# Optimization experiments

Measured on AMD Instinct MI355X. Metric: run time of the kernel, lower is better.

The kernel has to match this reference:

```python
import jax, jax.numpy as jnp
import numpy as np

B, T, C = 8, 2048, 2048   # batch, seq, embedding
A = 2048                  # attn_dim
H, N = 32, 64             # heads, head_size
LORA_MIX, LORA_DEC = 32, 64
EPS = 1e-5 * 8 ** 2       # GroupNorm eps with head_size_divisor=8


def setup_inputs() -> dict:
    key = jax.random.key(0)
    ks = jax.random.split(key, 24)
    s = lambda k, shape, scale=1.0: jax.random.normal(k, shape, jnp.float32) * scale
    inp = {
        'x': s(ks[0], (B, T, C)),
        'time_maa_x': jax.random.uniform(ks[1], (1, 1, C)),
        'time_maa_w': jax.random.uniform(ks[2], (1, 1, C)),
        'time_maa_k': jax.random.uniform(ks[3], (1, 1, C)),
        'time_maa_v': jax.random.uniform(ks[4], (1, 1, C)),
        'time_maa_r': jax.random.uniform(ks[5], (1, 1, C)),
        'time_maa_g': jax.random.uniform(ks[6], (1, 1, C)),
        'maa_w1': s(ks[7], (C, LORA_MIX * 5), 0.01),
        'maa_w2': s(ks[8], (5, LORA_MIX, C), 0.01),
        'time_decay': s(ks[9], (1, 1, A)) - 4.0,   # decay_speed init is in [-6,-1]
        'decay_w1': s(ks[10], (C, LORA_DEC), 0.01),
        'decay_w2': s(ks[11], (LORA_DEC, A), 0.01),
        'u': s(ks[12], (H, N), 0.1),
        'Wr': s(ks[13], (A, C), C ** -0.5),
        'Wk': s(ks[14], (A, C), C ** -0.5),
        'Wv': s(ks[15], (A, C), C ** -0.5),
        'Wg': s(ks[16], (A, C), C ** -0.5),
        'Wo': s(ks[17], (C, A), A ** -0.5),
        'ln_w': jnp.ones((A,), jnp.float32),
        'ln_b': jnp.zeros((A,), jnp.float32),
    }
    return inp


def wkv6(r, k, v, dec, u):
    # r,k,v,dec: (B,T,A) -> (T,B,H,N); dec already exp(-exp(w))
    def to_tbhn(a):
        return a.reshape(B, T, H, N).transpose(1, 0, 2, 3)
    rr, kk, vv, dd = map(to_tbhn, (r, k, v, dec))

    def step(S, inp):  # S: (B,H,N,N) indexed [key_chan i, val_chan j]
        rt, kt, vt, dt = inp
        a = kt[..., :, None] * vt[..., None, :]            # rank-1 update (B,H,N,N)
        y = jnp.einsum('bhi,bhij->bhj', rt, S + u[None, :, :, None] * a)
        S = dt[..., None] * S + a                          # per-key-channel decay
        return S, y

    S0 = jnp.zeros((B, H, N, N), r.dtype)
    _, y = jax.lax.scan(step, S0, (rr, kk, vv, dd))
    return y.transpose(1, 0, 2, 3).reshape(B, T, A)


def reference(x, time_maa_x, time_maa_w, time_maa_k, time_maa_v, time_maa_r,
              time_maa_g, maa_w1, maa_w2, time_decay, decay_w1, decay_w2,
              u, Wr, Wk, Wv, Wg, Wo, ln_w, ln_b):
    # token shift: x[t-1] - x[t] (zero-padded at t=0)
    xx = jnp.pad(x, ((0, 0), (1, 0), (0, 0)))[:, :T] - x
    xxx = x + xx * time_maa_x
    m = jnp.tanh(xxx @ maa_w1).reshape(B, T, 5, LORA_MIX)
    m = jnp.einsum('btfd,fdc->fbtc', m, maa_w2)            # (5,B,T,C)
    mw, mk, mv, mr, mg = m

    xw = x + xx * (time_maa_w + mw)
    xk = x + xx * (time_maa_k + mk)
    xv = x + xx * (time_maa_v + mv)
    xr = x + xx * (time_maa_r + mr)
    xg = x + xx * (time_maa_g + mg)

    r = xr @ Wr.T
    k = xk @ Wk.T
    v = xv @ Wv.T
    g = jax.nn.silu(xg @ Wg.T)
    w = time_decay + jnp.tanh(xw @ decay_w1) @ decay_w2
    dec = jnp.exp(-jnp.exp(w))                              # RWKV6 decay mapping

    y = wkv6(r, k, v, dec, u)

    # GroupNorm over each head's N channels
    yg = y.reshape(B, T, H, N)
    mu = yg.mean(-1, keepdims=True)
    var = yg.var(-1, keepdims=True)
    yn = ((yg - mu) * jax.lax.rsqrt(var + EPS)).reshape(B, T, A)
    yn = yn * ln_w + ln_b

    return (yn * g) @ Wo.T
```

## Files before the change

kernel.cpp:

```cpp
#include <hip/hip_runtime.h>
#include <hip/hip_bf16.h>
#include <cstdint>
#include <cstddef>

#define B_ 8
#define T_ 2048
#define C_ 2048
#define A_ 2048
#define H_ 32
#define BT_ (B_*T_)

typedef short short8 __attribute__((ext_vector_type(8)));
typedef _Float16 half8 __attribute__((ext_vector_type(8)));
typedef float floatx4 __attribute__((ext_vector_type(4)));

__device__ __forceinline__ unsigned short f2bf(float f) {
  union { float f; uint32_t u; } a; a.f = f;
  uint32_t r = a.u + 0x7fffu + ((a.u >> 16) & 1u);
  return (unsigned short)(r >> 16);
}
__device__ __forceinline__ float bf2f(unsigned short s) {
  union { uint32_t u; float f; } a; a.u = ((uint32_t)s) << 16;
  return a.f;
}
__device__ __forceinline__ unsigned short f2h(float f) {
  union { _Float16 h; unsigned short u; } c; c.h = (_Float16)f; return c.u;
}
__device__ __forceinline__ float h2f(unsigned short u) {
  union { unsigned short u; _Float16 h; } c; c.u = u; return (float)c.h;
}
__device__ __forceinline__ void split_hl(float v, unsigned short& hh, unsigned short& ll) {
  hh = f2bf(v);
  ll = f2bf(v - bf2f(hh));
}
__device__ __forceinline__ int swz(int row, int col) {
  return row * 64 + (col ^ ((row & 7) << 3));
}
__device__ __forceinline__ short8 ldfrag(const unsigned short* M, int row, int col8) {
  return *(const short8*)&M[row * 64 + (col8 ^ ((row & 7) << 3))];
}

__global__ void conv_f16(const float* __restrict__ s, unsigned short* __restrict__ d, int n) {
  int i = blockIdx.x * 256 + threadIdx.x;
  if (i < n) d[i] = f2h(s[i]);
}

__global__ void transpose_pad(const float* __restrict__ s, unsigned short* __restrict__ d, int NP, int NV) {
  int i = blockIdx.x * 256 + threadIdx.x;
  int n = i >> 11, kk = i & 2047;
  if (n < NP) d[i] = (n < NV) ? f2h(s[kk * NV + n]) : (unsigned short)0;
}

__global__ void transpose_w2(const float* __restrict__ s, unsigned short* __restrict__ d) {
  int i = blockIdx.x * 256 + threadIdx.x;
  int f = i >> 16, rem = i & 65535;
  int dd = rem >> 11, c = rem & 2047;
  d[((size_t)(f * 2048 + c) << 5) + dd] = f2h(s[((size_t)(f * 32 + dd) << 11) + c]);
}

__global__ void shift_mix(const float* __restrict__ x, const float* __restrict__ tmx,
                          unsigned short* __restrict__ xxx) {
  size_t i4 = (size_t)blockIdx.x * 256 + threadIdx.x;
  size_t i = i4 * 4;
  int c = (int)(i & 2047);
  int t = (int)((i >> 11) & 2047);
  float4 xv = *(const float4*)&x[i];
  float4 pv = make_float4(0.f, 0.f, 0.f, 0.f);
  if (t > 0) pv = *(const float4*)&x[i - 2048];
  float4 tv = *(const float4*)&tmx[c];
  ushort4 m;
  m.x = f2h(xv.x + (pv.x - xv.x) * tv.x);
  m.y = f2h(xv.y + (pv.y - xv.y) * tv.y);
  m.z = f2h(xv.z + (pv.z - xv.z) * tv.z);
  m.w = f2h(xv.w + (pv.w - xv.w) * tv.w);
  *(ushort4*)&xxx[i] = m;
}

__device__ __forceinline__ void gll16(const void* g, void* l) {
  __builtin_amdgcn_global_load_lds(
      (const __attribute__((address_space(1))) void*)g,
      (__attribute__((address_space(3))) void*)l, 16, 0, 0);
}

template<int EPI>
__global__ __launch_bounds__(256)
void gemm_f16(const unsigned short* __restrict__ Am, const unsigned short* __restrict__ Bm,
              void* __restrict__ Cp, int M, int N, int K) {
  __shared__ unsigned short As[128 * 32];
  __shared__ unsigned short Bs[128 * 32];
  const int tid = threadIdx.x;
  const int wid = tid >> 6, lane = tid & 63;
  const int quad = lane >> 4, l15 = lane & 15;
  const long bm = (long)blockIdx.x * 128, bn = (long)blockIdx.y * 128;
  const int wm = (wid & 1) * 64, wn = (wid >> 1) * 64;

  floatx4 acc[4][4];
#pragma unroll
  for (int a = 0; a < 4; a++)
#pragma unroll
    for (int b = 0; b < 4; b++) { floatx4 z = {0.f, 0.f, 0.f, 0.f}; acc[a][b] = z; }

  const int stg_row = wid * 32 + (lane >> 2);
  const int stg_k   = (lane & 3) * 8;
  const int stg_lds = wid * 1024 + lane * 8;

  for (int k0 = 0; k0 < K; k0 += 32) {
    __syncthreads();
#pragma unroll
    for (int p = 0; p < 2; ++p) {
      gll16(Am + (bm + stg_row + p * 16) * (long)K + k0 + stg_k, &As[stg_lds + p * 512]);
      gll16(Bm + (bn + stg_row + p * 16) * (long)K + k0 + stg_k, &Bs[stg_lds + p * 512]);
    }
    __syncthreads();

    half8 af[4], bfr[4];
#pragma unroll
    for (int mi = 0; mi < 4; mi++) af[mi] = *(const half8*)&As[(wm + mi * 16 + l15) * 32 + quad * 8];
#pragma unroll
    for (int ni = 0; ni < 4; ni++) bfr[ni] = *(const half8*)&Bs[(wn + ni * 16 + l15) * 32 + quad * 8];
#pragma unroll
    for (int mi = 0; mi < 4; mi++)
#pragma unroll
      for (int ni = 0; ni < 4; ni++)
        acc[mi][ni] = __builtin_amdgcn_mfma_f32_16x16x32_f16(af[mi], bfr[ni], acc[mi][ni], 0, 0, 0);
  }

#pragma unroll
  for (int mi = 0; mi < 4; mi++)
#pragma unroll
    for (int ni = 0; ni < 4; ni++)
#pragma unroll
      for (int vv = 0; vv < 4; ++vv) {
        long row = bm + wm + mi * 16 + quad * 4 + vv;
        long col = bn + wn + ni * 16 + l15;
        float val = acc[mi][ni][vv];
        if (EPI == 0) {
          ((unsigned short*)Cp)[row * N + col] = f2bf(val);
        } else if (EPI == 1) {
          float s = val / (1.f + __expf(-val));
          ((unsigned short*)Cp)[row * N + col] = f2h(s);
        } else if (EPI == 2) {
          ((float*)Cp)[row * N + col] = tanhf(val);
        } else if (EPI == 4) {
          ((unsigned short*)Cp)[row * N + col] = f2h(tanhf(val));
        } else {
          ((float*)Cp)[row * N + col] = val;
        }
      }
}

__global__ __launch_bounds__(256)
void mix_gemm(const unsigned short* __restrict__ m5f, const unsigned short* __restrict__ w2T,
              const float* __restrict__ x,
              const float* __restrict__ tmw, const float* __restrict__ tmk,
              const float* __restrict__ tmv, const float* __restrict__ tmr,
              const float* __restrict__ tmg,
              unsigned short* __restrict__ xw, unsigned short* __restrict__ xk,
              unsigned short* __restrict__ xv, unsigned short* __restrict__ xr,
              unsigned short* __restrict__ xg) {
  __shared__ unsigned short As[128 * 32];
  __shared__ unsigned short Bs[128 * 32];
  const int tid = threadIdx.x;
  const int wid = tid >> 6, lane = tid & 63;
  const int quad = lane >> 4, l15 = lane & 15;
  const long bm = (long)blockIdx.x * 128, bn = (long)blockIdx.y * 128;
  const int f = blockIdx.z;
  const int wm = (wid & 1) * 64, wn = (wid >> 1) * 64;

  const float* tmf = (f == 0) ? tmw : (f == 1) ? tmk : (f == 2) ? tmv : (f == 3) ? tmr : tmg;
  unsigned short* outf = (f == 0) ? xw : (f == 1) ? xk : (f == 2) ? xv : (f == 3) ? xr : xg;

  const int stg_row = wid * 32 + (lane >> 2);
  const int stg_k   = (lane & 3) * 8;
  const int stg_lds = wid * 1024 + lane * 8;

#pragma unroll
  for (int p = 0; p < 2; ++p) {
    gll16(m5f + (bm + stg_row + p * 16) * 256 + f * 32 + stg_k, &As[stg_lds + p * 512]);
    gll16(w2T + ((long)f * 2048 + bn + stg_row + p * 16) * 32 + stg_k, &Bs[stg_lds + p * 512]);
  }
  __syncthreads();

  half8 af[4], bfr[4];
#pragma unroll
  for (int mi = 0; mi < 4; mi++) af[mi] = *(const half8*)&As[(wm + mi * 16 + l15) * 32 + quad * 8];
#pragma unroll
  for (int ni = 0; ni < 4; ni++) bfr[ni] = *(const half8*)&Bs[(wn + ni * 16 + l15) * 32 + quad * 8];

  floatx4 acc[4][4];
#pragma unroll
  for (int a = 0; a < 4; a++)
#pragma unroll
    for (int b = 0; b < 4; b++) { floatx4 z = {0.f, 0.f, 0.f, 0.f}; acc[a][b] = z; }
#pragma unroll
  for (int mi = 0; mi < 4; mi++)
#pragma unroll
    for (int ni = 0; ni < 4; ni++)
      acc[mi][ni] = __builtin_amdgcn_mfma_f32_16x16x32_f16(af[mi], bfr[ni], acc[mi][ni], 0, 0, 0);

#pragma unroll
  for (int ni = 0; ni < 4; ni++) {
    const long col = bn + wn + ni * 16 + l15;
    const float tv = tmf[col];
#pragma unroll
    for (int mi = 0; mi < 4; mi++) {
      const long row0 = bm + wm + mi * 16 + quad * 4;
      const size_t idx0 = (size_t)row0 * 2048 + col;
      float xc[4];
#pragma unroll
      for (int vv = 0; vv < 4; ++vv) xc[vv] = x[idx0 + (size_t)vv * 2048];
      float xprev = ((row0 & 2047) > 0) ? x[idx0 - 2048] : 0.f;
#pragma unroll
      for (int vv = 0; vv < 4; ++vv) {
        const float xp = vv ? xc[vv - 1] : xprev;
        outf[idx0 + (size_t)vv * 2048] = f2h(xc[vv] + (xp - xc[vv]) * (tv + acc[mi][ni][vv]));
      }
    }
  }
}

__global__ __launch_bounds__(256)
void decay_kernel(const float* __restrict__ t1, const float* __restrict__ w2d,
                  const float* __restrict__ td, float* __restrict__ dec) {
  const int bt0 = blockIdx.x * 16;
  const int tid = threadIdx.x;
  for (int cc = 0; cc < 8; ++cc) {
    const int a = cc * 256 + tid;
    const float tda = td[a];
    float acc[16];
#pragma unroll
    for (int b = 0; b < 16; b++) acc[b] = 0.f;
    for (int dc = 0; dc < 16; ++dc) {
      float wv0 = w2d[((size_t)(dc * 4 + 0) << 11) + a];
      float wv1 = w2d[((size_t)(dc * 4 + 1) << 11) + a];
      float wv2 = w2d[((size_t)(dc * 4 + 2) << 11) + a];
      float wv3 = w2d[((size_t)(dc * 4 + 3) << 11) + a];
#pragma unroll
      for (int b = 0; b < 16; b++) {
        float4 mv = *(const float4*)&t1[((size_t)(bt0 + b) << 7) + dc * 4];
        acc[b] += mv.x * wv0 + mv.y * wv1 + mv.z * wv2 + mv.w * wv3;
      }
    }
#pragma unroll
    for (int b = 0; b < 16; b++) {
      dec[((size_t)(bt0 + b) << 11) + a] = __expf(-__expf(tda + acc[b]));
    }
  }
}

template<int KF32>
__global__ __launch_bounds__(512, 1)
void wkv6_chunk(const unsigned short* __restrict__ r, const unsigned short* __restrict__ k16,
                const float* __restrict__ k32, const float* __restrict__ v,
                const float* __restrict__ dec, const float* __restrict__ u,
                unsigned short* __restrict__ gz,
                const float* __restrict__ lnw, const float* __restrict__ lnb) {
  __shared__ unsigned short Rh[4096], Rl[4096];
  __shared__ unsigned short Kh[4096], Kl[4096];
  __shared__ unsigned short KTh[4096], KTl[4096];
  __shared__ unsigned short VTh[4096], VTl[4096];
  __shared__ unsigned short Amh[4096], Aml[4096];
  __shared__ unsigned short SThi[4096], STlo[4096];
  __shared__ float STf[4096];
  __shared__ float qpart[8][64];
  __shared__ float LcEnd[64];
  __shared__ float diagv[64];
  __shared__ float gnp[8][16][2];

  const int bh = blockIdx.x, b = bh >> 5, h = bh & 31;
  const int tid = threadIdx.x;
  const int w = tid >> 6, lane = tid & 63;
  const int quad = lane >> 4, l15 = lane & 15;
  const int cb = h * 64;
  const int wr = w >> 1, wc = w & 1;
  const int rq = w * 8;
  const int mrow = wr * 16;
  const int mcol = wc * 32;

  const float uu = u[cb + lane];
  float lnwv[2], lnbv[2];
#pragma unroll
  for (int ni = 0; ni < 2; ++ni) {
    lnwv[ni] = lnw[cb + mcol + ni * 16 + l15];
    lnbv[ni] = lnb[cb + mcol + ni * 16 + l15];
  }

  for (int i = tid; i < 4096; i += 512) STf[i] = 0.f;

  const size_t bT = (size_t)b * T_;

  float dA[8], rA[8], kA[8], vA[8];
  {
    const size_t ro = (bT + rq) * (size_t)A_ + cb + lane;
#pragma unroll
    for (int q = 0; q < 8; ++q) {
      const size_t o = ro + (size_t)q * A_;
      dA[q] = dec[o];
      rA[q] = bf2f(r[o]);
      if (KF32) kA[q] = k32[o];
      else      kA[q] = bf2f(k16[o]);
      vA[q] = v[o];
    }
  }

  for (int c = 0; c < T_ / 64; ++c) {
    const int t0 = c * 64;
    float lcq[8];
    lcq[0] = dA[0];
#pragma unroll
    for (int q = 1; q < 8; ++q) lcq[q] = lcq[q - 1] * dA[q];
    qpart[w][lane] = lcq[7];
    __syncthreads();
    {
      float pre = 1.f;
#pragma unroll
      for (int pw = 0; pw < 7; ++pw)
        if (pw < w) pre *= qpart[pw][lane];
      if (w == 7) LcEnd[lane] = pre * lcq[7];
      unsigned short hh, ll;
#pragma unroll
      for (int q = 0; q < 8; ++q) {
        const int jr = rq + q;
        split_hl(STf[jr * 64 + lane], hh, ll);
        const int ixs = swz(jr, lane);
        SThi[ixs] = hh; STlo[ixs] = ll;
      }
      short8 ktph, ktpl, vtph, vtpl;
#pragma unroll
      for (int q = 0; q < 8; ++q) {
        const int tr = rq + q;
        const float Pl = q ? pre * lcq[q - 1] : pre;
        const float Lc = pre * lcq[q];
        const int ix = swz(tr, lane);
        split_hl(rA[q] * Pl, hh, ll);
        Rh[ix] = hh; Rl[ix] = ll;
        const float kn = kA[q] / Lc;
        split_hl(kn, hh, ll);
        Kh[ix] = hh; Kl[ix] = ll;
        ktph[q] = (short)hh; ktpl[q] = (short)ll;
        split_hl(vA[q], hh, ll);
        vtph[q] = (short)hh; vtpl[q] = (short)ll;
        float dp = rA[q] * uu * kA[q];
        dp += __shfl_xor(dp, 1, 64);
        dp += __shfl_xor(dp, 2, 64);
        dp += __shfl_xor(dp, 4, 64);
        dp += __shfl_xor(dp, 8, 64);
        dp += __shfl_xor(dp, 16, 64);
        dp += __shfl_xor(dp, 32, 64);
        if (lane == 0) diagv[tr] = dp;
      }
      const int ixT = lane * 64 + (rq ^ ((lane & 7) << 3));
      *(short8*)&KTh[ixT] = ktph;
      *(short8*)&KTl[ixT] = ktpl;
      *(short8*)&VTh[ixT] = vtph;
      *(short8*)&VTl[ixT] = vtpl;
    }
    __syncthreads();
    if (c + 1 < T_ / 64) {
      const size_t ro = (bT + t0 + 64 + rq) * (size_t)A_ + cb + lane;
#pragma unroll
      for (int q = 0; q < 8; ++q) {
        const size_t o = ro + (size_t)q * A_;
        dA[q] = dec[o];
        rA[q] = bf2f(r[o]);
        if (KF32) kA[q] = k32[o];
        else      kA[q] = bf2f(k16[o]);
        vA[q] = v[o];
      }
    }
    {
      short8 arh[2], arl[2];
#pragma unroll
      for (int kst = 0; kst < 2; ++kst) {
        const int c8 = kst * 32 + quad * 8;
        arh[kst] = ldfrag(Rh, mrow + l15, c8);
        arl[kst] = ldfrag(Rl, mrow + l15, c8);
      }
      floatx4 acc[2];
#pragma unroll
      for (int ni = 0; ni < 2; ++ni) { floatx4 z = {0.f, 0.f, 0.f, 0.f}; acc[ni] = z; }
#pragma unroll
      for (int ni = 0; ni < 2; ++ni)
#pragma unroll
        for (int kst = 0; kst < 2; ++kst) {
          const int c8 = kst * 32 + quad * 8;
          short8 bh_ = ldfrag(Kh, mcol + ni * 16 + l15, c8);
          short8 bl_ = ldfrag(Kl, mcol + ni * 16 + l15, c8);
          acc[ni] = __builtin_amdgcn_mfma_f32_16x16x32_bf16(arh[kst], bh_, acc[ni], 0, 0, 0);
          acc[ni] = __builtin_amdgcn_mfma_f32_16x16x32_bf16(arh[kst], bl_, acc[ni], 0, 0, 0);
          acc[ni] = __builtin_amdgcn_mfma_f32_16x16x32_bf16(arl[kst], bh_, acc[ni], 0, 0, 0);
        }
#pragma unroll
      for (int ni = 0; ni < 2; ++ni)
#pragma unroll
        for (int vv = 0; vv < 4; ++vv) {
          const int grow = mrow + quad * 4 + vv;
          const int gcol = mcol + ni * 16 + l15;
          float val = (grow > gcol) ? acc[ni][vv] : ((grow == gcol) ? diagv[grow] : 0.f);
          unsigned short hh, ll;
          split_hl(val, hh, ll);
          const int ix = swz(grow, gcol);
          Amh[ix] = hh; Aml[ix] = ll;
        }
    }
    __syncthreads();
    {
      short8 aAh[2], aAl[2], aRh[2], aRl[2];
#pragma unroll
      for (int kst = 0; kst < 2; ++kst) {
        const int c8 = kst * 32 + quad * 8;
        aAh[kst] = ldfrag(Amh, mrow + l15, c8);
        aAl[kst] = ldfrag(Aml, mrow + l15, c8);
        aRh[kst] = ldfrag(Rh, mrow + l15, c8);
        aRl[kst] = ldfrag(Rl, mrow + l15, c8);
      }
      floatx4 acc[2];
#pragma unroll
      for (int ni = 0; ni < 2; ++ni) { floatx4 z = {0.f, 0.f, 0.f, 0.f}; acc[ni] = z; }
#pragma unroll
      for (int ni = 0; ni < 2; ++ni)
#pragma unroll
        for (int kst = 0; kst < 2; ++kst) {
          const int c8 = kst * 32 + quad * 8;
          const int brow = mcol + ni * 16 + l15;
          short8 bvh = ldfrag(VTh, brow, c8);
          short8 bvl = ldfrag(VTl, brow, c8);
          acc[ni] = __builtin_amdgcn_mfma_f32_16x16x32_bf16(aAh[kst], bvh, acc[ni], 0, 0, 0);
          acc[ni] = __builtin_amdgcn_mfma_f32_16x16x32_bf16(aAh[kst], bvl, acc[ni], 0, 0, 0);
          acc[ni] = __builtin_amdgcn_mfma_f32_16x16x32_bf16(aAl[kst], bvh, acc[ni], 0, 0, 0);
          short8 bsh = ldfrag(SThi, brow, c8);
          short8 bsl = ldfrag(STlo, brow, c8);
          acc[ni] = __builtin_amdgcn_mfma_f32_16x16x32_bf16(aRh[kst], bsh, acc[ni], 0, 0, 0);
          acc[ni] = __builtin_amdgcn_mfma_f32_16x16x32_bf16(aRh[kst], bsl, acc[ni], 0, 0, 0);
          acc[ni] = __builtin_amdgcn_mfma_f32_16x16x32_bf16(aRl[kst], bsh, acc[ni], 0, 0, 0);
        }
      float s1_[4], s2_[4];
#pragma unroll
      for (int vv = 0; vv < 4; ++vv) {
        float s1 = acc[0][vv] + acc[1][vv];
        float s2 = acc[0][vv] * acc[0][vv] + acc[1][vv] * acc[1][vv];
        s1 += __shfl_xor(s1, 1, 64); s2 += __shfl_xor(s2, 1, 64);
        s1 += __shfl_xor(s1, 2, 64); s2 += __shfl_xor(s2, 2, 64);
        s1 += __shfl_xor(s1, 4, 64); s2 += __shfl_xor(s2, 4, 64);
        s1 += __shfl_xor(s1, 8, 64); s2 += __shfl_xor(s2, 8, 64);
        s1_[vv] = s1; s2_[vv] = s2;
        if (l15 == 0) {
          gnp[w][quad * 4 + vv][0] = s1;
          gnp[w][quad * 4 + vv][1] = s2;
        }
      }
      __syncthreads();
#pragma unroll
      for (int ni = 0; ni < 2; ++ni)
#pragma unroll
        for (int vv = 0; vv < 4; ++vv) {
          const int rloc = quad * 4 + vv;
          float s1 = s1_[vv] + gnp[w ^ 1][rloc][0];
          float s2 = s2_[vv] + gnp[w ^ 1][rloc][1];
          float mu = s1 * (1.f / 64.f);
          float var = s2 * (1.f / 64.f) - mu * mu;
          float rs = rsqrtf(var + 6.4e-4f);
          const size_t off = (bT + t0 + mrow + rloc) * (size_t)A_ + cb + mcol + ni * 16 + l15;
          float yn = (acc[ni][vv] - mu) * rs * lnwv[ni] + lnbv[ni];
          float z = yn * h2f(gz[off]);
          gz[off] = f2h(z);
        }
    }
    {
      short8 avh[2], avl[2];
#pragma unroll
      for (int kst = 0; kst < 2; ++kst) {
        const int c8 = kst * 32 + quad * 8;
        avh[kst] = ldfrag(VTh, mrow + l15, c8);
        avl[kst] = ldfrag(VTl, mrow + l15, c8);
      }
      floatx4 a4[2];
#pragma unroll
      for (int ni = 0; ni < 2; ++ni) { floatx4 z = {0.f, 0.f, 0.f, 0.f}; a4[ni] = z; }
#pragma unroll
      for (int ni = 0; ni < 2; ++ni)
#pragma unroll
        for (int kst = 0; kst < 2; ++kst) {
          const int c8 = kst * 32 + quad * 8;
          short8 bkh = ldfrag(KTh, mcol + ni * 16 + l15, c8);
          short8 bkl = ldfrag(KTl, mcol + ni * 16 + l15, c8);
          a4[ni] = __builtin_amdgcn_mfma_f32_16x16x32_bf16(avh[kst], bkh, a4[ni], 0, 0, 0);
          a4[ni] = __builtin_amdgcn_mfma_f32_16x16x32_bf16(avh[kst], bkl, a4[ni], 0, 0, 0);
          a4[ni] = __builtin_amdgcn_mfma_f32_16x16x32_bf16(avl[kst], bkh, a4[ni], 0, 0, 0);
        }
#pragma unroll
      for (int ni = 0; ni < 2; ++ni) {
        const float lce = LcEnd[mcol + ni * 16 + l15];
#pragma unroll
        for (int vv = 0; vv < 4; ++vv) {
          const int jr = mrow + quad * 4 + vv;
          const int ic = mcol + ni * 16 + l15;
          STf[jr * 64 + ic] = lce * (a4[ni][vv] + STf[jr * 64 + ic]);
        }
      }
    }
    __syncthreads();
  }
}

extern "C" void kernel_launch(void* const* d_in, const int* in_sizes, int n_in,
                              void* d_out, int out_size, void* d_ws, size_t ws_size,
                              hipStream_t stream) {
  (void)in_sizes; (void)n_in; (void)out_size;
  const float* x   = (const float*)d_in[0];
  const float* tmx = (const float*)d_in[1];
  const float* tmw = (const float*)d_in[2];
  const float* tmk = (const float*)d_in[3];
  const float* tmv = (const float*)d_in[4];
  const float* tmr = (const float*)d_in[5];
  const float* tmg = (const float*)d_in[6];
  const float* w1  = (const float*)d_in[7];
  const float* w2  = (const float*)d_in[8];
  const float* td  = (const float*)d_in[9];
  const float* dw1 = (const float*)d_in[10];
  const float* dw2 = (const float*)d_in[11];
  const float* u   = (const float*)d_in[12];
  const float* Wr  = (const float*)d_in[13];
  const float* Wk  = (const float*)d_in[14];
  const float* Wv  = (const float*)d_in[15];
  const float* Wg  = (const float*)d_in[16];
  const float* Wo  = (const float*)d_in[17];
  const float* lnw = (const float*)d_in[18];
  const float* lnb = (const float*)d_in[19];

  char* ws = (char*)d_ws;
  const size_t MB = 1024 * 1024;
  unsigned short* xxx  = (unsigned short*)(ws + 0 * MB);
  unsigned short* gb   = (unsigned short*)(ws + 0 * MB);
  unsigned short* m5   = (unsigned short*)(ws + 64 * MB);
  float*          vf   = (float*)(ws + 64 * MB);
  unsigned short* w1T  = (unsigned short*)(ws + 128 * MB);
  unsigned short* bxk  = (unsigned short*)(ws + 128 * MB);
  unsigned short* bxv  = (unsigned short*)(ws + 192 * MB);
  float*          decb = (float*)(ws + 192 * MB);
  unsigned short* bxw  = (unsigned short*)(ws + 256 * MB);
  unsigned short* bxg  = (unsigned short*)(ws + 320 * MB);
  unsigned short* rb   = (unsigned short*)(ws + 320 * MB);
  unsigned short* bxr  = (unsigned short*)(ws + 384 * MB);
  unsigned short* kb   = (unsigned short*)(ws + 384 * MB);
  unsigned short* dw1T = (unsigned short*)(ws + 448 * MB);
  unsigned short* Wf   = (unsigned short*)(ws + 448 * MB);
  unsigned short* w2T  = (unsigned short*)(ws + 460 * MB);
  float*          t1   = (float*)(ws + 464 * MB);
  const bool kf32 = ws_size >= (size_t)616 * MB;
  float* kf = (float*)(ws + 480 * MB);

  const int nW = A_ * C_;
  const size_t EBT = (size_t)BT_ * C_;

  shift_mix<<<(int)(EBT / 4 / 256), 256, 0, stream>>>(x, tmx, xxx);

  transpose_pad<<<(256 * 2048) / 256, 256, 0, stream>>>(w1, w1T, 256, 160);
  gemm_f16<4><<<dim3(BT_ / 128, 2), 256, 0, stream>>>(xxx, w1T, m5, BT_, 256, 2048);

  transpose_w2<<<(5 * 65536) / 256, 256, 0, stream>>>(w2, w2T);
  mix_gemm<<<dim3(BT_ / 128, C_ / 128, 5), 256, 0, stream>>>(m5, w2T, x,
                                                             tmw, tmk, tmv, tmr, tmg,
                                                             bxw, bxk, bxv, bxr, bxg);

  transpose_pad<<<(128 * 2048) / 256, 256, 0, stream>>>(dw1, dw1T, 128, 64);
  gemm_f16<2><<<dim3(BT_ / 128, 1), 256, 0, stream>>>(bxw, dw1T, t1, BT_, 128, 2048);

  conv_f16<<<nW / 256, 256, 0, stream>>>(Wg, Wf, nW);
  gemm_f16<1><<<dim3(BT_ / 128, 16), 256, 0, stream>>>(bxg, Wf, gb, BT_, 2048, 2048);
  conv_f16<<<nW / 256, 256, 0, stream>>>(Wr, Wf, nW);
  gemm_f16<0><<<dim3(BT_ / 128, 16), 256, 0, stream>>>(bxr, Wf, rb, BT_, 2048, 2048);
  conv_f16<<<nW / 256, 256, 0, stream>>>(Wk, Wf, nW);
  if (kf32) {
    gemm_f16<3><<<dim3(BT_ / 128, 16), 256, 0, stream>>>(bxk, Wf, kf, BT_, 2048, 2048);
  } else {
    gemm_f16<0><<<dim3(BT_ / 128, 16), 256, 0, stream>>>(bxk, Wf, kb, BT_, 2048, 2048);
  }
  conv_f16<<<nW / 256, 256, 0, stream>>>(Wv, Wf, nW);
  gemm_f16<3><<<dim3(BT_ / 128, 16), 256, 0, stream>>>(bxv, Wf, vf, BT_, 2048, 2048);

  decay_kernel<<<BT_ / 16, 256, 0, stream>>>(t1, dw2, td, decb);

  if (kf32) {
    wkv6_chunk<1><<<256, 512, 0, stream>>>(rb, kb, kf, vf, decb, u, gb, lnw, lnb);
  } else {
    wkv6_chunk<0><<<256, 512, 0, stream>>>(rb, kb, kf, vf, decb, u, gb, lnw, lnb);
  }

  conv_f16<<<nW / 256, 256, 0, stream>>>(Wo, Wf, nW);
  gemm_f16<3><<<dim3(BT_ / 128, 16), 256, 0, stream>>>(gb, Wf, (float*)d_out, BT_, 2048, 2048);
}
```

Baseline: 2.095 ms.

## Add 256x256-tile GEMM with 4-stage async LDS pipeline for projections

Introduces a new f16 MFMA GEMM kernel using 256x256 block tiles, 512 threads, a 4-buffer direct global-to-LDS pipeline with XOR-swizzled shared memory, and priority hints around the MFMA bursts. All five large 2048x2048 projection GEMMs (g, r, k, v, output) switch to it. The aim is higher arithmetic intensity per block and better overlap of loads with compute. The cost is much more register and LDS pressure, which can reduce occupancy. With 512 blocks the grid is also coarser.

Result: faster. 2.013 ms (-3.9%).

```diff
diff --git a/kernel.cpp b/kernel.cpp
--- a/kernel.cpp
+++ b/kernel.cpp
@@ -147,6 +147,119 @@
           ((float*)Cp)[row * N + col] = val;
         }
       }
+}
+
+template<int EPI>
+__global__ __launch_bounds__(512, 2)
+void gemm256(const unsigned short* __restrict__ Am, const unsigned short* __restrict__ Bm,
+             void* __restrict__ Cp, int M, int N, int K) {
+  __shared__ unsigned short At[4][8192];
+  __shared__ unsigned short Bt[4][8192];
+  const int tid = threadIdx.x;
+  const int w = tid >> 6, lane = tid & 63;
+  const int quad = lane >> 4, l15 = lane & 15;
+  const long bm = (long)blockIdx.x * 256, bn = (long)blockIdx.y * 256;
+  const int wm = (w & 1) * 128, wn = (w >> 1) * 64;
+
+  floatx4 acc[8][4];
+#pragma unroll
+  for (int a = 0; a < 8; a++)
+#pragma unroll
+    for (int b = 0; b < 4; b++) { floatx4 z = {0.f, 0.f, 0.f, 0.f}; acc[a][b] = z; }
+
+  int srow[2], scol[2];
+#pragma unroll
+  for (int u = 0; u < 2; ++u) {
+    int p = u * 8192 + tid * 16;
+    int l = p ^ (((p >> 6) & 3) << 4);
+    srow[u] = l >> 6;
+    scol[u] = (l & 63) >> 1;
+  }
+  const int ldst = tid * 16;
+
+  const int NT = K >> 5;
+  for (int t = 0; t < 3; ++t) {
+#pragma unroll
+    for (int u = 0; u < 2; ++u) {
+      gll16(Am + (bm + srow[u]) * (long)K + (t << 5) + scol[u],
+            (char*)&At[t][0] + u * 8192 + ldst);
+      gll16(Bm + (bn + srow[u]) * (long)K + (t << 5) + scol[u],
+            (char*)&Bt[t][0] + u * 8192 + ldst);
+    }
+  }
+  asm volatile("s_waitcnt vmcnt(8) lgkmcnt(0)\n\ts_barrier" ::: "memory");
+
+  for (int t = 0; t < NT; ++t) {
+    const int bi = t & 3;
+    const unsigned short* Ab = At[bi];
+    const unsigned short* Bb = Bt[bi];
+    const int tn = t + 3;
+    const bool do_stage = tn < NT;
+    const int bj = tn & 3;
+
+    if (do_stage) {
+      gll16(Am + (bm + srow[0]) * (long)K + (tn << 5) + scol[0], (char*)&At[bj][0] + ldst);
+      gll16(Bm + (bn + srow[0]) * (long)K + (tn << 5) + scol[0], (char*)&Bt[bj][0] + ldst);
+    }
+    half8 bfr[4], af[4];
+#pragma unroll
+    for (int ni = 0; ni < 4; ++ni) {
+      int r = wn + ni * 16 + l15;
+      bfr[ni] = *(const half8*)((const char*)Bb + r * 64 + ((quad ^ (r & 3)) << 4));
+    }
+#pragma unroll
+    for (int mi = 0; mi < 4; ++mi) {
+      int r = wm + mi * 16 + l15;
+      af[mi] = *(const half8*)((const char*)Ab + r * 64 + ((quad ^ (r & 3)) << 4));
+    }
+    __builtin_amdgcn_s_setprio(1);
+#pragma unroll
+    for (int mi = 0; mi < 4; ++mi)
+#pragma unroll
+      for (int ni = 0; ni < 4; ++ni)
+        acc[mi][ni] = __builtin_amdgcn_mfma_f32_16x16x32_f16(af[mi], bfr[ni], acc[mi][ni], 0, 0, 0);
+    __builtin_amdgcn_s_setprio(0);
+
+    if (do_stage) {
+      gll16(Am + (bm + srow[1]) * (long)K + (tn << 5) + scol[1], (char*)&At[bj][0] + 8192 + ldst);
+      gll16(Bm + (bn + srow[1]) * (long)K + (tn << 5) + scol[1], (char*)&Bt[bj][0] + 8192 + ldst);
+    }
+#pragma unroll
+    for (int mi = 0; mi < 4; ++mi) {
+      int r = wm + 64 + mi * 16 + l15;
+      af[mi] = *(const half8*)((const char*)Ab + r * 64 + ((quad ^ (r & 3)) << 4));
+    }
+    __builtin_amdgcn_s_setprio(1);
+#pragma unroll
+    for (int mi = 0; mi < 4; ++mi)
+#pragma unroll
+      for (int ni = 0; ni < 4; ++ni)
+        acc[4 + mi][ni] = __builtin_amdgcn_mfma_f32_16x16x32_f16(af[mi], bfr[ni], acc[4 + mi][ni], 0, 0, 0);
+    __builtin_amdgcn_s_setprio(0);
+
+    asm volatile("s_waitcnt vmcnt(8) lgkmcnt(0)\n\ts_barrier" ::: "memory");
+  }
+
+#pragma unroll
+  for (int p = 0; p < 2; ++p)
+#pragma unroll
+    for (int mi = 0; mi < 4; ++mi)
+#pragma unroll
+      for (int ni = 0; ni < 4; ++ni)
+#pragma unroll
+        for (int vv = 0; vv < 4; ++vv) {
+          long row = bm + wm + p * 64 + mi * 16 + quad * 4 + vv;
+          long col = bn + wn + ni * 16 + l15;
+          float val = acc[p * 4 + mi][ni][vv];
+          if (EPI == 0) {
+            ((unsigned short*)Cp)[row * N + col] = f2bf(val);
+          } else if (EPI == 1) {
+            float s = val / (1.f + __expf(-val));
+            ((unsigned short*)Cp)[row * N + col] = f2h(s);
+          } else {
+            ((float*)Cp)[row * N + col] = val;
+          }
+        }
 }
 
 __global__ __launch_bounds__(256)
@@ -567,17 +680,17 @@
   gemm_f16<2><<<dim3(BT_ / 128, 1), 256, 0, stream>>>(bxw, dw1T, t1, BT_, 128, 2048);
 
   conv_f16<<<nW / 256, 256, 0, stream>>>(Wg, Wf, nW);
-  gemm_f16<1><<<dim3(BT_ / 128, 16), 256, 0, stream>>>(bxg, Wf, gb, BT_, 2048, 2048);
+  gemm256<1><<<dim3(BT_ / 256, C_ / 256), 512, 0, stream>>>(bxg, Wf, gb, BT_, 2048, 2048);
   conv_f16<<<nW / 256, 256, 0, stream>>>(Wr, Wf, nW);
-  gemm_f16<0><<<dim3(BT_ / 128, 16), 256, 0, stream>>>(bxr, Wf, rb, BT_, 2048, 2048);
+  gemm256<0><<<dim3(BT_ / 256, C_ / 256), 512, 0, stream>>>(bxr, Wf, rb, BT_, 2048, 2048);
   conv_f16<<<nW / 256, 256, 0, stream>>>(Wk, Wf, nW);
   if (kf32) {
-    gemm_f16<3><<<dim3(BT_ / 128, 16), 256, 0, stream>>>(bxk, Wf, kf, BT_, 2048, 2048);
+    gemm256<3><<<dim3(BT_ / 256, C_ / 256), 512, 0, stream>>>(bxk, Wf, kf, BT_, 2048, 2048);
   } else {
-    gemm_f16<0><<<dim3(BT_ / 128, 16), 256, 0, stream>>>(bxk, Wf, kb, BT_, 2048, 2048);
+    gemm256<0><<<dim3(BT_ / 256, C_ / 256), 512, 0, stream>>>(bxk, Wf, kb, BT_, 2048, 2048);
   }
   conv_f16<<<nW / 256, 256, 0, stream>>>(Wv, Wf, nW);
-  gemm_f16<3><<<dim3(BT_ / 128, 16), 256, 0, stream>>>(bxv, Wf, vf, BT_, 2048, 2048);
+  gemm256<3><<<dim3(BT_ / 256, C_ / 256), 512, 0, stream>>>(bxv, Wf, vf, BT_, 2048, 2048);
 
   decay_kernel<<<BT_ / 16, 256, 0, stream>>>(t1, dw2, td, decb);
 
@@ -588,5 +701,5 @@
   }
 
   conv_f16<<<nW / 256, 256, 0, stream>>>(Wo, Wf, nW);
-  gemm_f16<3><<<dim3(BT_ / 128, 16), 256, 0, stream>>>(gb, Wf, (float*)d_out, BT_, 2048, 2048);
-}
+  gemm256<3><<<dim3(BT_ / 256, C_ / 256), 512, 0, stream>>>(gb, Wf, (float*)d_out, BT_, 2048, 2048);
+}
```
